# Kernel optimization log

Hardware: AMD Instinct MI355X
Metric: run time of the kernel (lower is better)

Reference implementation:

```python
import jax, jax.numpy as jnp
import numpy as np

B, S, V, D, L, H = 2, 512, 100300, 768, 12, 3072


def setup_inputs() -> dict:
    key = jax.random.key(0)
    ks = jax.random.split(key, 24)
    nrm = lambda k, shape, s=0.02: (jax.random.normal(k, shape, jnp.float32) * s)
    uni = lambda k, shape: jax.random.uniform(k, shape, jnp.float32)
    return {
        "tokens": jax.random.randint(ks[0], (B, S), 0, V, dtype=jnp.int32),
        "emb": nrm(ks[1], (V, D)),
        "ln0_g": jnp.ones((D,), jnp.float32), "ln0_b": jnp.zeros((D,), jnp.float32),
        "ln1_g": jnp.ones((L, D), jnp.float32), "ln1_b": jnp.zeros((L, D), jnp.float32),
        "ln2_g": jnp.ones((L, D), jnp.float32), "ln2_b": jnp.zeros((L, D), jnp.float32),
        "time_decay": nrm(ks[2], (L, D), 0.5),
        "time_first": nrm(ks[3], (L, D), 0.5),
        "tm_mu_k": uni(ks[4], (L, D)), "tm_mu_v": uni(ks[5], (L, D)), "tm_mu_r": uni(ks[6], (L, D)),
        "tm_Wk": nrm(ks[7], (L, D, D)), "tm_Wv": nrm(ks[8], (L, D, D)),
        "tm_Wr": nrm(ks[9], (L, D, D)), "tm_Wo": nrm(ks[10], (L, D, D)),
        "cm_mu_k": uni(ks[11], (L, D)), "cm_mu_r": uni(ks[12], (L, D)),
        "cm_Wk": nrm(ks[13], (L, D, H)), "cm_Wv": nrm(ks[14], (L, H, D)), "cm_Wr": nrm(ks[15], (L, D, D)),
        "lnf_g": jnp.ones((D,), jnp.float32), "lnf_b": jnp.zeros((D,), jnp.float32),
        "head": nrm(ks[16], (D, V)),
    }


def _ln(x, g, b, eps=1e-5):
    m = jnp.mean(x, axis=-1, keepdims=True)
    v = jnp.mean(jnp.square(x - m), axis=-1, keepdims=True)
    return (x - m) * jax.lax.rsqrt(v + eps) * g + b


def _shift(x):  # previous-token shift along seq axis, zeros at t=0; x: [B,S,D]
    return jnp.concatenate([jnp.zeros_like(x[:, :1]), x[:, :-1]], axis=1)


def _wkv(k, v, w, u):
    """RWKV-4 max-stabilized WKV linear recurrence. k,v: [B,S,D]; w,u: [D]."""
    decay = -jnp.exp(w)  # negative per-channel decay

    def step(carry, inp):
        p, a, b = carry
        kt, vt = inp
        ww = u + kt
        q = jnp.maximum(p, ww)
        e1 = jnp.exp(p - q)
        e2 = jnp.exp(ww - q)
        out = (e1 * a + e2 * vt) / (e1 * b + e2)
        ww2 = p + decay
        q2 = jnp.maximum(ww2, kt)
        e1 = jnp.exp(ww2 - q2)
        e2 = jnp.exp(kt - q2)
        return (q2, e1 * a + e2 * vt, e1 * b + e2), out

    kT = jnp.swapaxes(k, 0, 1)  # [S,B,D]
    vT = jnp.swapaxes(v, 0, 1)
    p0 = jnp.full((k.shape[0], k.shape[2]), -1e38, k.dtype)
    a0 = jnp.zeros_like(p0)
    b0 = jnp.zeros_like(p0)
    _, out = jax.lax.scan(step, (p0, a0, b0), (kT, vT))
    return jnp.swapaxes(out, 0, 1)  # [B,S,D]


def reference(tokens, emb, ln0_g, ln0_b, ln1_g, ln1_b, ln2_g, ln2_b,
              time_decay, time_first, tm_mu_k, tm_mu_v, tm_mu_r,
              tm_Wk, tm_Wv, tm_Wr, tm_Wo, cm_mu_k, cm_mu_r,
              cm_Wk, cm_Wv, cm_Wr, lnf_g, lnf_b, head):
    x = emb[tokens]                      # [B,S,D]
    x = _ln(x, ln0_g, ln0_b)
    n_layer = ln1_g.shape[0]
    for l in range(n_layer):
        # --- time mixing ---
        xx = _ln(x, ln1_g[l], ln1_b[l])
        sx = _shift(xx)
        xk = xx * tm_mu_k[l] + sx * (1.0 - tm_mu_k[l])
        xv = xx * tm_mu_v[l] + sx * (1.0 - tm_mu_v[l])
        xr = xx * tm_mu_r[l] + sx * (1.0 - tm_mu_r[l])
        r = jax.nn.sigmoid(jnp.einsum('bsd,de->bse', xr, tm_Wr[l]))
        k = jnp.einsum('bsd,de->bse', xk, tm_Wk[l])
        v = jnp.einsum('bsd,de->bse', xv, tm_Wv[l])
        wkv = _wkv(k, v, time_decay[l], time_first[l])
        x = x + jnp.einsum('bsd,de->bse', r * wkv, tm_Wo[l])
        # --- channel mixing ---
        xx = _ln(x, ln2_g[l], ln2_b[l])
        sx = _shift(xx)
        xk = xx * cm_mu_k[l] + sx * (1.0 - cm_mu_k[l])
        xr = xx * cm_mu_r[l] + sx * (1.0 - cm_mu_r[l])
        kk = jnp.square(jax.nn.relu(jnp.einsum('bsd,dh->bsh', xk, cm_Wk[l])))
        x = x + jax.nn.sigmoid(jnp.einsum('bsd,de->bse', xr, cm_Wr[l])) * jnp.einsum('bsh,hd->bsd', kk, cm_Wv[l])
    x = _ln(x, lnf_g, lnf_b)
    return jnp.einsum('bsd,dv->bsv', x, head)  # [B,S,V] logits
```

## Files before the change

### kernel.cpp

```cpp
#include <hip/hip_runtime.h>

typedef float f32x4v __attribute__((ext_vector_type(4)));
typedef __bf16 bf16x8 __attribute__((ext_vector_type(8)));

__device__ __forceinline__ ushort f2bf(float f) {
    unsigned u = __builtin_bit_cast(unsigned, f);
    return (ushort)((u + 0x7FFFu + ((u >> 16) & 1u)) >> 16);
}

__device__ __forceinline__ void gload16(const void* g, void* l) {
    __builtin_amdgcn_global_load_lds(
        (const __attribute__((address_space(1))) void*)g,
        (__attribute__((address_space(3))) void*)l, 16, 0, 0);
}

__global__ __launch_bounds__(256)
void prep_w(const float* __restrict__ Win, ushort* __restrict__ Wout,
            int K, int N, size_t sIn, size_t sOut)
{
    __shared__ float t[64][65];
    const float* W = Win + sIn * blockIdx.z;
    ushort* O = Wout + sOut * blockIdx.z;
    int n0 = blockIdx.x * 64, k0 = blockIdx.y * 64;
    int tid = threadIdx.x;
    int c = tid & 63, r4 = tid >> 6;
#pragma unroll
    for (int i = 0; i < 16; i++) {
        int rr = i * 4 + r4;
        int n = n0 + c;
        t[rr][c] = (n < N) ? W[(size_t)(k0 + rr) * N + n] : 0.f;
    }
    __syncthreads();
#pragma unroll
    for (int i = 0; i < 16; i++) {
        int nr = i * 4 + r4;
        O[(size_t)(n0 + nr) * K + k0 + c] = f2bf(t[c][nr]);
    }
}

__global__ __launch_bounds__(256)
void prep_dd(const float* __restrict__ W0, const float* __restrict__ W1,
             const float* __restrict__ W2, const float* __restrict__ W3,
             const float* __restrict__ W4,
             ushort* __restrict__ O0, ushort* __restrict__ O1,
             ushort* __restrict__ O2, ushort* __restrict__ O3,
             ushort* __restrict__ O4)
{
    __shared__ float t[64][65];
    const int z = blockIdx.z, wsel = z / 12, l = z % 12;
    const size_t DD = (size_t)768 * 768;
    const float* W = (wsel == 0 ? W0 : wsel == 1 ? W1 : wsel == 2 ? W2 : wsel == 3 ? W3 : W4) + DD * l;
    ushort* O = (wsel == 0 ? O0 : wsel == 1 ? O1 : wsel == 2 ? O2 : wsel == 3 ? O3 : O4) + DD * l;
    int n0 = blockIdx.x * 64, k0 = blockIdx.y * 64;
    int tid = threadIdx.x;
    int c = tid & 63, r4 = tid >> 6;
#pragma unroll
    for (int i = 0; i < 16; i++) {
        int rr = i * 4 + r4;
        t[rr][c] = W[(size_t)(k0 + rr) * 768 + n0 + c];
    }
    __syncthreads();
#pragma unroll
    for (int i = 0; i < 16; i++) {
        int nr = i * 4 + r4;
        O[(size_t)(n0 + nr) * 768 + k0 + c] = f2bf(t[c][nr]);
    }
}

template <int BM, int BN, int EPI>
__device__ __forceinline__
void gemm_body(const ushort* __restrict__ A, const ushort* __restrict__ B,
               float* __restrict__ C, ushort* __restrict__ Obf,
               const float* __restrict__ G,
               int N, int K, int mtiles, int bid, int tid,
               ushort* __restrict__ As, ushort* __restrict__ Bs)
{
    constexpr int WM = BM / 2, WN = BN / 2, MF = WM / 16, NF = WN / 16;
    const int mt = bid % mtiles, nt = bid / mtiles;
    const int m0 = mt * BM, n0 = nt * BN;
    const int w = tid >> 6, l = tid & 63;
    const int wr = w >> 1, wc = w & 1, g = l >> 4, lr = l & 15;
    const int lrow = l >> 3, lcol = ((l & 7) ^ lrow) * 8;

    auto stage = [&](int buf, int k0) {
#pragma unroll
        for (int i = 0; i < BM / 32; i++) {
            int rb = (i * 4 + w) * 8;
            gload16(A + (size_t)(m0 + rb + lrow) * K + k0 + lcol, &As[buf * BM * 64 + rb * 64]);
        }
#pragma unroll
        for (int i = 0; i < BN / 32; i++) {
            int rb = (i * 4 + w) * 8;
            gload16(B + (size_t)(n0 + rb + lrow) * K + k0 + lcol, &Bs[buf * BN * 64 + rb * 64]);
        }
    };

    f32x4v acc[MF][NF] = {};
    auto comp = [&](int buf) {
#pragma unroll
        for (int kk = 0; kk < 2; kk++) {
            bf16x8 af[MF], bfr[NF];
            const int sl = ((kk * 4 + g) ^ (lr & 7)) * 8;
#pragma unroll
            for (int mi = 0; mi < MF; mi++)
                af[mi] = *(const bf16x8*)&As[buf * BM * 64 + (wr * WM + mi * 16 + lr) * 64 + sl];
#pragma unroll
            for (int ni = 0; ni < NF; ni++)
                bfr[ni] = *(const bf16x8*)&Bs[buf * BN * 64 + (wc * WN + ni * 16 + lr) * 64 + sl];
#pragma unroll
            for (int mi = 0; mi < MF; mi++)
#pragma unroll
                for (int ni = 0; ni < NF; ni++)
                    acc[mi][ni] = __builtin_amdgcn_mfma_f32_16x16x32_bf16(
                        af[mi], bfr[ni], acc[mi][ni], 0, 0, 0);
        }
    };

    const int NS = K >> 6;
    stage(0, 0);
    __syncthreads();
    for (int s = 0; s < NS; s++) {
        if (s + 1 < NS) stage((s + 1) & 1, (s + 1) << 6);
        comp(s & 1);
        __syncthreads();
    }

#pragma unroll
    for (int mi = 0; mi < MF; mi++) {
        int row = m0 + wr * WM + mi * 16 + 4 * g;
#pragma unroll
        for (int ni = 0; ni < NF; ni++) {
            int col = n0 + wc * WN + ni * 16 + lr;
#pragma unroll
            for (int q = 0; q < 4; q++) {
                size_t idx = (size_t)(row + q) * N + col;
                float vv = acc[mi][ni][q];
                if constexpr (EPI == 0) {
                    C[idx] = vv;
                } else if constexpr (EPI == 1) {
                    C[idx] += vv;
                } else if constexpr (EPI == 2) {
                    float t = vv > 0.f ? vv : 0.f;
                    Obf[idx] = f2bf(t * t);
                } else {
                    float gt = 1.f / (1.f + __expf(-G[idx]));
                    C[idx] += gt * vv;
                }
            }
        }
    }
}

template <int BM, int BN, int EPI>
__global__ __launch_bounds__(256)
void gemm2(const ushort* __restrict__ Abase,
           const ushort* __restrict__ B0, const ushort* __restrict__ B1,
           const ushort* __restrict__ B2,
           float* __restrict__ Cbase, ushort* __restrict__ ObfBase,
           const float* __restrict__ Gbase,
           int M, int N, int K, int mtiles)
{
    __shared__ ushort As[2 * BM * 64];
    __shared__ ushort Bs[2 * BN * 64];
    const int z = blockIdx.z;
    const ushort* A = Abase + (size_t)z * M * K;
    const ushort* B = (z == 0) ? B0 : ((z == 1) ? B1 : B2);
    float* C = Cbase ? Cbase + (size_t)z * M * N : nullptr;
    ushort* Obf = ObfBase ? ObfBase + (size_t)z * M * N : nullptr;
    int bid = blockIdx.x;
    { int cpx = gridDim.x >> 3; bid = (bid & 7) * cpx + (bid >> 3); }
    gemm_body<BM, BN, EPI>(A, B, C, Obf, Gbase, N, K, mtiles, bid, threadIdx.x, As, Bs);
}

__global__ __launch_bounds__(256)
void gemm_ckcr(const ushort* __restrict__ xk, const ushort* __restrict__ xr,
               const ushort* __restrict__ ckT, const ushort* __restrict__ crT,
               ushort* __restrict__ hbuf, float* __restrict__ rrb)
{
    __shared__ ushort As[2 * 64 * 64];
    __shared__ ushort Bs[2 * 32 * 64];
    int bid = blockIdx.x;
    { int cpx = gridDim.x >> 3; bid = (bid & 7) * cpx + (bid >> 3); }
    if (bid < 1536)
        gemm_body<64, 32, 2>(xk, ckT, nullptr, hbuf, nullptr, 3072, 768, 16,
                             bid, threadIdx.x, As, Bs);
    else
        gemm_body<64, 32, 0>(xr, crT, rrb, nullptr, nullptr, 768, 768, 16,
                             bid - 1536, threadIdx.x, As, Bs);
}

__global__ __launch_bounds__(256, 4)
void head_gemm(const ushort* __restrict__ A, const ushort* __restrict__ B,
               float* __restrict__ C, int M, int N, int K, int mtiles)
{
    constexpr int WM = 64, WN = 64;
    __shared__ ushort As[2][128 * 32];
    __shared__ ushort Bs[2][128 * 32];

    int bid = blockIdx.x;
    { int cpx = gridDim.x >> 3; bid = (bid & 7) * cpx + (bid >> 3); }
    const int mt = bid % mtiles, nt = bid / mtiles;
    const int m0 = mt * 128, n0 = nt * 128;
    const int tid = threadIdx.x, w = tid >> 6, l = tid & 63;
    const int wr = w >> 1, wc = w & 1, g = l >> 4, lr = l & 15;
    const int lrow = l >> 2;
    const int lcol = ((l & 3) ^ (lrow & 3) ^ ((lrow >> 2) & 3)) * 8;

    auto stage = [&](int buf, int k0) {
#pragma unroll
        for (int i = 0; i < 2; i++) {
            int rg = i * 4 + w;
            gload16(A + (size_t)(m0 + rg * 16 + lrow) * K + k0 + lcol, &As[buf][rg * 512]);
        }
#pragma unroll
        for (int i = 0; i < 2; i++) {
            int rg = i * 4 + w;
            gload16(B + (size_t)(n0 + rg * 16 + lrow) * K + k0 + lcol, &Bs[buf][rg * 512]);
        }
    };

    f32x4v acc[4][4] = {};
    auto comp = [&](int buf) {
        bf16x8 af[4], bfr[4];
        const int sl = (g ^ (lr & 3) ^ ((lr >> 2) & 3)) * 8;
#pragma unroll
        for (int mi = 0; mi < 4; mi++)
            af[mi] = *(const bf16x8*)&As[buf][(wr * WM + mi * 16 + lr) * 32 + sl];
#pragma unroll
        for (int ni = 0; ni < 4; ni++)
            bfr[ni] = *(const bf16x8*)&Bs[buf][(wc * WN + ni * 16 + lr) * 32 + sl];
#pragma unroll
        for (int mi = 0; mi < 4; mi++)
#pragma unroll
            for (int ni = 0; ni < 4; ni++)
                acc[mi][ni] = __builtin_amdgcn_mfma_f32_16x16x32_bf16(
                    af[mi], bfr[ni], acc[mi][ni], 0, 0, 0);
    };

    const int NS = K / 32;
    stage(0, 0);
    __syncthreads();
    for (int s = 0; s < NS; s++) {
        if (s + 1 < NS) stage((s + 1) & 1, (s + 1) * 32);
        comp(s & 1);
        __syncthreads();
    }

#pragma unroll
    for (int mi = 0; mi < 4; mi++) {
        int row = m0 + wr * WM + mi * 16 + 4 * g;
#pragma unroll
        for (int ni = 0; ni < 4; ni++) {
            int col = n0 + wc * WN + ni * 16 + lr;
            if (col >= N) continue;
#pragma unroll
            for (int q = 0; q < 4; q++)
                C[(size_t)(row + q) * N + col] = acc[mi][ni][q];
        }
    }
}

__device__ __forceinline__ float4 blockReduce4(float4 v) {
#pragma unroll
    for (int off = 32; off; off >>= 1) {
        v.x += __shfl_down(v.x, off);
        v.y += __shfl_down(v.y, off);
        v.z += __shfl_down(v.z, off);
        v.w += __shfl_down(v.w, off);
    }
    __shared__ float4 red[4];
    int tid = threadIdx.x;
    if ((tid & 63) == 0) red[tid >> 6] = v;
    __syncthreads();
    float4 r = red[0];
    r.x += red[1].x + red[2].x + red[3].x;
    r.y += red[1].y + red[2].y + red[3].y;
    r.z += red[1].z + red[2].z + red[3].z;
    r.w += red[1].w + red[2].w + red[3].w;
    return r;
}

__global__ void embed_ln0(const int* __restrict__ tokens, const float* __restrict__ emb,
                          const float* __restrict__ g, const float* __restrict__ be,
                          float* __restrict__ x)
{
    int tau = blockIdx.x, tid = threadIdx.x;
    const float* e = emb + (size_t)tokens[tau] * 768;
    float a[3]; float s1 = 0, s2 = 0;
#pragma unroll
    for (int i = 0; i < 3; i++) {
        float av = e[tid + i * 256]; a[i] = av; s1 += av; s2 += av * av;
    }
    float4 r = blockReduce4(make_float4(s1, s2, 0.f, 0.f));
    const float inv = 1.f / 768.f;
    float m = r.x * inv, va = r.y * inv - m * m, rs = rsqrtf(va + 1e-5f);
#pragma unroll
    for (int i = 0; i < 3; i++) {
        int d = tid + i * 256;
        x[(size_t)tau * 768 + d] = (a[i] - m) * rs * g[d] + be[d];
    }
}

__global__ void ln_mix_tm(const float* __restrict__ x,
                          const float* __restrict__ g, const float* __restrict__ be,
                          const float* __restrict__ muk, const float* __restrict__ muv,
                          const float* __restrict__ mur,
                          ushort* __restrict__ xk, ushort* __restrict__ xv,
                          ushort* __restrict__ xr)
{
    int tau = blockIdx.x, tid = threadIdx.x;
    bool hasp = (tau & 511) != 0;
    const float* xp = x + (size_t)tau * 768;
    const float* pp = xp - 768;
    float a[3], b[3]; float s1 = 0, s2 = 0, s3 = 0, s4 = 0;
#pragma unroll
    for (int i = 0; i < 3; i++) {
        int d = tid + i * 256;
        float av = xp[d]; a[i] = av; s1 += av; s2 += av * av;
        float bv = hasp ? pp[d] : 0.f; b[i] = bv; s3 += bv; s4 += bv * bv;
    }
    float4 r = blockReduce4(make_float4(s1, s2, s3, s4));
    const float inv = 1.f / 768.f;
    float m1 = r.x * inv, va = r.y * inv - m1 * m1, rs1 = rsqrtf(va + 1e-5f);
    float m2 = r.z * inv, vb = r.w * inv - m2 * m2, rs2 = rsqrtf(vb + 1e-5f);
#pragma unroll
    for (int i = 0; i < 3; i++) {
        int d = tid + i * 256;
        float gg = g[d], bb = be[d];
        float xx = (a[i] - m1) * rs1 * gg + bb;
        float sx = hasp ? ((b[i] - m2) * rs2 * gg + bb) : 0.f;
        size_t o = (size_t)tau * 768 + d;
        float mk = muk[d]; xk[o] = f2bf(xx * mk + sx * (1.f - mk));
        float mv = muv[d]; xv[o] = f2bf(xx * mv + sx * (1.f - mv));
        float mr = mur[d]; xr[o] = f2bf(xx * mr + sx * (1.f - mr));
    }
}

__global__ void ln_mix_cm(const float* __restrict__ x,
                          const float* __restrict__ g, const float* __restrict__ be,
                          const float* __restrict__ muk, const float* __restrict__ mur,
                          ushort* __restrict__ xk, ushort* __restrict__ xr)
{
    int tau = blockIdx.x, tid = threadIdx.x;
    bool hasp = (tau & 511) != 0;
    const float* xp = x + (size_t)tau * 768;
    const float* pp = xp - 768;
    float a[3], b[3]; float s1 = 0, s2 = 0, s3 = 0, s4 = 0;
#pragma unroll
    for (int i = 0; i < 3; i++) {
        int d = tid + i * 256;
        float av = xp[d]; a[i] = av; s1 += av; s2 += av * av;
        float bv = hasp ? pp[d] : 0.f; b[i] = bv; s3 += bv; s4 += bv * bv;
    }
    float4 r = blockReduce4(make_float4(s1, s2, s3, s4));
    const float inv = 1.f / 768.f;
    float m1 = r.x * inv, va = r.y * inv - m1 * m1, rs1 = rsqrtf(va + 1e-5f);
    float m2 = r.z * inv, vb = r.w * inv - m2 * m2, rs2 = rsqrtf(vb + 1e-5f);
#pragma unroll
    for (int i = 0; i < 3; i++) {
        int d = tid + i * 256;
        float gg = g[d], bb = be[d];
        float xx = (a[i] - m1) * rs1 * gg + bb;
        float sx = hasp ? ((b[i] - m2) * rs2 * gg + bb) : 0.f;
        size_t o = (size_t)tau * 768 + d;
        float mk = muk[d]; xk[o] = f2bf(xx * mk + sx * (1.f - mk));
        float mr = mur[d]; xr[o] = f2bf(xx * mr + sx * (1.f - mr));
    }
}

__global__ void ln_final(const float* __restrict__ x,
                         const float* __restrict__ g, const float* __restrict__ be,
                         ushort* __restrict__ xf)
{
    int tau = blockIdx.x, tid = threadIdx.x;
    const float* xp = x + (size_t)tau * 768;
    float a[3]; float s1 = 0, s2 = 0;
#pragma unroll
    for (int i = 0; i < 3; i++) {
        float av = xp[tid + i * 256]; a[i] = av; s1 += av; s2 += av * av;
    }
    float4 r = blockReduce4(make_float4(s1, s2, 0.f, 0.f));
    const float inv = 1.f / 768.f;
    float m = r.x * inv, va = r.y * inv - m * m, rs = rsqrtf(va + 1e-5f);
#pragma unroll
    for (int i = 0; i < 3; i++) {
        int d = tid + i * 256;
        xf[(size_t)tau * 768 + d] = f2bf((a[i] - m) * rs * g[d] + be[d]);
    }
}

__global__ __launch_bounds__(256)
void wkv_par(const float* __restrict__ kk, const float* __restrict__ vv,
             const float* __restrict__ rr, const float* __restrict__ td,
             const float* __restrict__ tf, ushort* __restrict__ out)
{
    const int blk = blockIdx.x, tid = threadIdx.x;
    const int b = blk / 48, chb = blk % 48;
    const int seg = tid >> 4, ch = tid & 15;
    const int d = chb * 16 + ch;
    const size_t base = (size_t)b * 512 * 768 + d;
    const size_t soff = (size_t)seg * 32 * 768;
    const float w = -__expf(td[d]);
    const float u = tf[d];
    const int CH = 8;

    __shared__ float sp[240], sa[240], sb[240];
    __shared__ float pp[256], pa[256], pb[256];

    if (seg < 15) {
        float p = -1e38f, aa = 0.f, bb = 0.f;
        const float* kp = kk + base + soff;
        const float* vp = vv + base + soff;
        float k8[CH], v8[CH], kn[CH], vn[CH];
#pragma unroll
        for (int j = 0; j < CH; j++) { k8[j] = kp[j * 768]; v8[j] = vp[j * 768]; }
        for (int c = 0; c < 32 / CH; c++) {
            if (c + 1 < 32 / CH) {
                size_t o = (size_t)(c + 1) * CH * 768;
#pragma unroll
                for (int j = 0; j < CH; j++) { kn[j] = kp[o + j * 768]; vn[j] = vp[o + j * 768]; }
            }
#pragma unroll
            for (int j = 0; j < CH; j++) {
                float kt = k8[j], vt = v8[j];
                float ww2 = p + w;
                float q2 = fmaxf(ww2, kt);
                float f1 = __expf(ww2 - q2), f2 = __expf(kt - q2);
                aa = f1 * aa + f2 * vt;
                bb = f1 * bb + f2;
                p = q2;
            }
#pragma unroll
            for (int j = 0; j < CH; j++) { k8[j] = kn[j]; v8[j] = vn[j]; }
        }
        sp[seg * 16 + ch] = p; sa[seg * 16 + ch] = aa; sb[seg * 16 + ch] = bb;
    }
    __syncthreads();

    if (tid < 16) {
        const float shift = 32.f * w;
        float P = -1e38f, A = 0.f, Bc = 0.f;
#pragma unroll
        for (int s = 0; s < 16; s++) {
            pp[s * 16 + tid] = P; pa[s * 16 + tid] = A; pb[s * 16 + tid] = Bc;
            if (s < 15) {
                float ps = P + shift;
                float sps = sp[s * 16 + tid];
                float q = fmaxf(ps, sps);
                float e1 = __expf(ps - q), e2 = __expf(sps - q);
                A  = e1 * A  + e2 * sa[s * 16 + tid];
                Bc = e1 * Bc + e2 * sb[s * 16 + tid];
                P = q;
            }
        }
    }
    __syncthreads();

    {
        float p = pp[tid], aa = pa[tid], bb = pb[tid];
        const float* kp = kk + base + soff;
        const float* vp = vv + base + soff;
        const float* rp = rr + base + soff;
        ushort* op = out + base + soff;
        float k8[CH], v8[CH], r8[CH], kn[CH], vn[CH], rn[CH];
#pragma unroll
        for (int j = 0; j < CH; j++) {
            k8[j] = kp[j * 768]; v8[j] = vp[j * 768]; r8[j] = rp[j * 768];
        }
        for (int c = 0; c < 32 / CH; c++) {
            if (c + 1 < 32 / CH) {
                size_t o = (size_t)(c + 1) * CH * 768;
#pragma unroll
                for (int j = 0; j < CH; j++) {
                    kn[j] = kp[o + j * 768]; vn[j] = vp[o + j * 768]; rn[j] = rp[o + j * 768];
                }
            }
#pragma unroll
            for (int j = 0; j < CH; j++) {
                float kt = k8[j], vt = v8[j];
                float ww = u + kt;
                float q = fmaxf(p, ww);
                float e1 = __expf(p - q), e2 = __expf(ww - q);
                float o = (e1 * aa + e2 * vt) / (e1 * bb + e2);
                float sr = 1.f / (1.f + __expf(-r8[j]));
                op[(size_t)(c * CH + j) * 768] = f2bf(sr * o);
                float ww2 = p + w;
                float q2 = fmaxf(ww2, kt);
                float f1 = __expf(ww2 - q2), f2 = __expf(kt - q2);
                aa = f1 * aa + f2 * vt;
                bb = f1 * bb + f2;
                p = q2;
            }
#pragma unroll
            for (int j = 0; j < CH; j++) { k8[j] = kn[j]; v8[j] = vn[j]; r8[j] = rn[j]; }
        }
    }
}

extern "C" void kernel_launch(void* const* d_in, const int* in_sizes, int n_in,
                              void* d_out, int out_size, void* d_ws, size_t ws_size,
                              hipStream_t stream)
{
    const int V = 100300, D = 768, L = 12, H = 3072;
    const int T = 1024;
    const int Vp = 100352;

    const int*   tokens     = (const int*)d_in[0];
    const float* emb        = (const float*)d_in[1];
    const float* ln0_g      = (const float*)d_in[2];
    const float* ln0_b      = (const float*)d_in[3];
    const float* ln1_g      = (const float*)d_in[4];
    const float* ln1_b      = (const float*)d_in[5];
    const float* ln2_g      = (const float*)d_in[6];
    const float* ln2_b      = (const float*)d_in[7];
    const float* time_decay = (const float*)d_in[8];
    const float* time_first = (const float*)d_in[9];
    const float* tm_mu_k    = (const float*)d_in[10];
    const float* tm_mu_v    = (const float*)d_in[11];
    const float* tm_mu_r    = (const float*)d_in[12];
    const float* tm_Wk      = (const float*)d_in[13];
    const float* tm_Wv      = (const float*)d_in[14];
    const float* tm_Wr      = (const float*)d_in[15];
    const float* tm_Wo      = (const float*)d_in[16];
    const float* cm_mu_k    = (const float*)d_in[17];
    const float* cm_mu_r    = (const float*)d_in[18];
    const float* cm_Wk      = (const float*)d_in[19];
    const float* cm_Wv      = (const float*)d_in[20];
    const float* cm_Wr      = (const float*)d_in[21];
    const float* lnf_g      = (const float*)d_in[22];
    const float* lnf_b      = (const float*)d_in[23];
    const float* head       = (const float*)d_in[24];

    char* wp = (char*)d_ws;
    auto alloc = [&](size_t bytes) -> char* {
        char* p = wp; wp += (bytes + 255) & ~(size_t)255; return p;
    };
    const size_t eDD = (size_t)L * D * D;
    const size_t eDH = (size_t)L * D * H;
    ushort* wkT = (ushort*)alloc(eDD * 2);
    ushort* wvT = (ushort*)alloc(eDD * 2);
    ushort* wrT = (ushort*)alloc(eDD * 2);
    ushort* woT = (ushort*)alloc(eDD * 2);
    ushort* ckT = (ushort*)alloc(eDH * 2);
    ushort* cvT = (ushort*)alloc(eDH * 2);
    ushort* crT = (ushort*)alloc(eDD * 2);
    ushort* hdT = (ushort*)alloc((size_t)Vp * D * 2);

    float*  x    = (float*)alloc((size_t)T * D * 4);
    ushort* xkb  = (ushort*)alloc((size_t)3 * T * D * 2);
    float*  kvr  = (float*)alloc((size_t)3 * T * D * 4);
    ushort* rwkv = (ushort*)alloc((size_t)T * D * 2);
    ushort* hbuf = (ushort*)alloc((size_t)T * H * 2);
    float*  rrb  = (float*)alloc((size_t)T * D * 4);
    ushort* xf   = (ushort*)alloc((size_t)T * D * 2);

    prep_dd<<<dim3(12, 12, 60), 256, 0, stream>>>(tm_Wk, tm_Wv, tm_Wr, tm_Wo, cm_Wr,
                                                  wkT, wvT, wrT, woT, crT);
    prep_w<<<dim3(H / 64, D / 64, L), 256, 0, stream>>>(cm_Wk, ckT, D, H, (size_t)D * H, (size_t)D * H);
    prep_w<<<dim3(D / 64, H / 64, L), 256, 0, stream>>>(cm_Wv, cvT, H, D, (size_t)D * H, (size_t)D * H);
    prep_w<<<dim3(Vp / 64, D / 64, 1), 256, 0, stream>>>(head, hdT, D, V, 0, 0);

    embed_ln0<<<T, 256, 0, stream>>>(tokens, emb, ln0_g, ln0_b, x);

    for (int l = 0; l < L; l++) {
        ln_mix_tm<<<T, 256, 0, stream>>>(x, ln1_g + l * D, ln1_b + l * D,
                                         tm_mu_k + l * D, tm_mu_v + l * D, tm_mu_r + l * D,
                                         xkb, xkb + (size_t)T * D, xkb + (size_t)2 * T * D);

        gemm2<64, 32, 0><<<dim3(384, 1, 3), 256, 0, stream>>>(
            xkb, wkT + l * (size_t)D * D, wvT + l * (size_t)D * D, wrT + l * (size_t)D * D,
            kvr, nullptr, nullptr, T, D, D, 16);

        wkv_par<<<96, 256, 0, stream>>>(kvr, kvr + (size_t)T * D, kvr + (size_t)2 * T * D,
                                        time_decay + l * D, time_first + l * D, rwkv);

        gemm2<64, 32, 1><<<dim3(384, 1, 1), 256, 0, stream>>>(
            rwkv, woT + l * (size_t)D * D, nullptr, nullptr,
            x, nullptr, nullptr, T, D, D, 16);

        ln_mix_cm<<<T, 256, 0, stream>>>(x, ln2_g + l * D, ln2_b + l * D,
                                         cm_mu_k + l * D, cm_mu_r + l * D,
                                         xkb, xkb + (size_t)T * D);

        gemm_ckcr<<<1920, 256, 0, stream>>>(xkb, xkb + (size_t)T * D,
                                            ckT + l * (size_t)D * H, crT + l * (size_t)D * D,
                                            hbuf, rrb);

        gemm2<64, 32, 3><<<dim3(384, 1, 1), 256, 0, stream>>>(
            hbuf, cvT + l * (size_t)D * H, nullptr, nullptr,
            x, nullptr, rrb, T, D, H, 16);
    }

    ln_final<<<T, 256, 0, stream>>>(x, lnf_g, lnf_b, xf);

    head_gemm<<<8 * (Vp / 128), 256, 0, stream>>>(xf, hdT, (float*)d_out, T, V, D, 8);
}
```

Measured before the change: 1.875 ms.

## Rewrite head GEMM with 256x256 tiles, 8 waves, and quarter-tile staged pipeline

```diff
diff --git a/kernel.cpp b/kernel.cpp
--- a/kernel.cpp
+++ b/kernel.cpp
@@ -189,73 +189,94 @@
                              bid - 1536, threadIdx.x, As, Bs);
 }
 
-__global__ __launch_bounds__(256, 4)
-void head_gemm(const ushort* __restrict__ A, const ushort* __restrict__ B,
-               float* __restrict__ C, int M, int N, int K, int mtiles)
-{
-    constexpr int WM = 64, WN = 64;
-    __shared__ ushort As[2][128 * 32];
-    __shared__ ushort Bs[2][128 * 32];
+#define HG_NT 12
+__global__ __launch_bounds__(512, 2)
+void head_gemm8(const ushort* __restrict__ Ag, const ushort* __restrict__ Bg,
+                float* __restrict__ C, int N)
+{
+    __shared__ ushort As[2][256 * 64];
+    __shared__ ushort Bs[2][256 * 64];
 
     int bid = blockIdx.x;
     { int cpx = gridDim.x >> 3; bid = (bid & 7) * cpx + (bid >> 3); }
-    const int mt = bid % mtiles, nt = bid / mtiles;
-    const int m0 = mt * 128, n0 = nt * 128;
+    const int mt = bid % 4, nt = bid / 4;
+    const int m0 = mt * 256, n0 = nt * 256;
     const int tid = threadIdx.x, w = tid >> 6, l = tid & 63;
-    const int wr = w >> 1, wc = w & 1, g = l >> 4, lr = l & 15;
-    const int lrow = l >> 2;
-    const int lcol = ((l & 3) ^ (lrow & 3) ^ ((lrow >> 2) & 3)) * 8;
-
-    auto stage = [&](int buf, int k0) {
-#pragma unroll
-        for (int i = 0; i < 2; i++) {
-            int rg = i * 4 + w;
-            gload16(A + (size_t)(m0 + rg * 16 + lrow) * K + k0 + lcol, &As[buf][rg * 512]);
-        }
-#pragma unroll
-        for (int i = 0; i < 2; i++) {
-            int rg = i * 4 + w;
-            gload16(B + (size_t)(n0 + rg * 16 + lrow) * K + k0 + lcol, &Bs[buf][rg * 512]);
+    const int wr = w >> 2, wc = w & 3, g = l >> 4, lr = l & 15;
+    const int lrow = l >> 3, lcol = ((l & 7) ^ lrow) * 8;
+
+    auto stageH = [&](int H) {
+        const int tau = H >> 2, part = H & 3, buf = tau & 1;
+        const int k0 = tau * 64;
+        const int half = (part >> 1) * 128;
+        ushort* dst;
+        const ushort* src;
+        int rbase;
+        if (part & 1) { dst = &Bs[buf][half * 64]; src = Bg; rbase = n0; }
+        else          { dst = &As[buf][half * 64]; src = Ag; rbase = m0; }
+#pragma unroll
+        for (int j = 0; j < 2; j++) {
+            int o = j * 8 + w;
+            gload16(src + (size_t)(rbase + half + o * 8 + lrow) * 768 + k0 + lcol,
+                    dst + o * 8 * 64);
         }
     };
 
-    f32x4v acc[4][4] = {};
-    auto comp = [&](int buf) {
-        bf16x8 af[4], bfr[4];
-        const int sl = (g ^ (lr & 3) ^ ((lr >> 2) & 3)) * 8;
-#pragma unroll
-        for (int mi = 0; mi < 4; mi++)
-            af[mi] = *(const bf16x8*)&As[buf][(wr * WM + mi * 16 + lr) * 32 + sl];
-#pragma unroll
-        for (int ni = 0; ni < 4; ni++)
-            bfr[ni] = *(const bf16x8*)&Bs[buf][(wc * WN + ni * 16 + lr) * 32 + sl];
-#pragma unroll
-        for (int mi = 0; mi < 4; mi++)
-#pragma unroll
-            for (int ni = 0; ni < 4; ni++)
-                acc[mi][ni] = __builtin_amdgcn_mfma_f32_16x16x32_bf16(
-                    af[mi], bfr[ni], acc[mi][ni], 0, 0, 0);
-    };
-
-    const int NS = K / 32;
-    stage(0, 0);
-    __syncthreads();
-    for (int s = 0; s < NS; s++) {
-        if (s + 1 < NS) stage((s + 1) & 1, (s + 1) * 32);
-        comp(s & 1);
-        __syncthreads();
-    }
-
-#pragma unroll
-    for (int mi = 0; mi < 4; mi++) {
-        int row = m0 + wr * WM + mi * 16 + 4 * g;
+    f32x4v acc[8][4] = {};
+
+#pragma unroll
+    for (int H = 0; H < 4; H++) stageH(H);
+
+    for (int t = 0; t < HG_NT; t++) {
+        const int buf = t & 1;
+#pragma unroll
+        for (int q = 0; q < 4; q++) {
+            __builtin_amdgcn_sched_barrier(0);
+            int H = 4 * t + q + 4;
+            if (H < 4 * HG_NT) stageH(H);
+            if (q == 0) {
+                if (t < HG_NT - 1) asm volatile("s_waitcnt vmcnt(2)" ::: "memory");
+                else               asm volatile("s_waitcnt vmcnt(0)" ::: "memory");
+            }
+            __builtin_amdgcn_s_barrier();
+            __builtin_amdgcn_sched_barrier(0);
+            __builtin_amdgcn_s_setprio(1);
+            {
+                const int mq = q >> 1, nq = q & 1;
+#pragma unroll
+                for (int kk = 0; kk < 2; kk++) {
+                    const int sl = ((kk * 4 + g) ^ (lr & 7)) * 8;
+                    bf16x8 af[4], bfr[2];
+#pragma unroll
+                    for (int i = 0; i < 4; i++)
+                        af[i] = *(const bf16x8*)&As[buf][(wr * 128 + (mq * 4 + i) * 16 + lr) * 64 + sl];
+#pragma unroll
+                    for (int j = 0; j < 2; j++)
+                        bfr[j] = *(const bf16x8*)&Bs[buf][(wc * 64 + (nq * 2 + j) * 16 + lr) * 64 + sl];
+#pragma unroll
+                    for (int i = 0; i < 4; i++)
+#pragma unroll
+                        for (int j = 0; j < 2; j++)
+                            acc[mq * 4 + i][nq * 2 + j] = __builtin_amdgcn_mfma_f32_16x16x32_bf16(
+                                af[i], bfr[j], acc[mq * 4 + i][nq * 2 + j], 0, 0, 0);
+                }
+            }
+            __builtin_amdgcn_s_setprio(0);
+            __builtin_amdgcn_sched_barrier(0);
+            __builtin_amdgcn_s_barrier();
+        }
+    }
+
+#pragma unroll
+    for (int mi = 0; mi < 8; mi++) {
+        int row = m0 + wr * 128 + mi * 16 + 4 * g;
 #pragma unroll
         for (int ni = 0; ni < 4; ni++) {
-            int col = n0 + wc * WN + ni * 16 + lr;
+            int col = n0 + wc * 64 + ni * 16 + lr;
             if (col >= N) continue;
 #pragma unroll
-            for (int q = 0; q < 4; q++)
-                C[(size_t)(row + q) * N + col] = acc[mi][ni][q];
+            for (int qq = 0; qq < 4; qq++)
+                C[(size_t)(row + qq) * N + col] = acc[mi][ni][qq];
         }
     }
 }
@@ -593,5 +614,5 @@
 
     ln_final<<<T, 256, 0, stream>>>(x, lnf_g, lnf_b, xf);
 
-    head_gemm<<<8 * (Vp / 128), 256, 0, stream>>>(xf, hdT, (float*)d_out, T, V, D, 8);
-}
+    head_gemm8<<<4 * (Vp / 256), 512, 0, stream>>>(xf, hdT, (float*)d_out, V);
+}
```

After: 1.980 ms. 5.6% more time.

## Software-pipeline head GEMM with split-K half-plane staging and explicit waitcnts

Applied to the files above, without the earlier changes.

```diff
diff --git a/kernel.cpp b/kernel.cpp
--- a/kernel.cpp
+++ b/kernel.cpp
@@ -189,69 +189,92 @@
                              bid - 1536, threadIdx.x, As, Bs);
 }
 
-__global__ __launch_bounds__(256, 4)
-void head_gemm(const ushort* __restrict__ A, const ushort* __restrict__ B,
-               float* __restrict__ C, int M, int N, int K, int mtiles)
-{
-    constexpr int WM = 64, WN = 64;
-    __shared__ ushort As[2][128 * 32];
-    __shared__ ushort Bs[2][128 * 32];
+#define HNT 12
+__global__ __launch_bounds__(256, 2)
+void head_gemmP(const ushort* __restrict__ Ag, const ushort* __restrict__ Bg,
+                float* __restrict__ C, int N)
+{
+    __shared__ ushort As[2][2][128 * 32];
+    __shared__ ushort Bs[2][2][128 * 32];
 
     int bid = blockIdx.x;
     { int cpx = gridDim.x >> 3; bid = (bid & 7) * cpx + (bid >> 3); }
-    const int mt = bid % mtiles, nt = bid / mtiles;
+    const int mt = bid % 8, nt = bid / 8;
     const int m0 = mt * 128, n0 = nt * 128;
     const int tid = threadIdx.x, w = tid >> 6, l = tid & 63;
     const int wr = w >> 1, wc = w & 1, g = l >> 4, lr = l & 15;
-    const int lrow = l >> 2;
-    const int lcol = ((l & 3) ^ (lrow & 3) ^ ((lrow >> 2) & 3)) * 8;
-
-    auto stage = [&](int buf, int k0) {
-#pragma unroll
-        for (int i = 0; i < 2; i++) {
-            int rg = i * 4 + w;
-            gload16(A + (size_t)(m0 + rg * 16 + lrow) * K + k0 + lcol, &As[buf][rg * 512]);
-        }
-#pragma unroll
-        for (int i = 0; i < 2; i++) {
-            int rg = i * 4 + w;
-            gload16(B + (size_t)(n0 + rg * 16 + lrow) * K + k0 + lcol, &Bs[buf][rg * 512]);
+    const int srow = l >> 2;
+    const int sslot = (l & 3) ^ ((l >> 2) & 3) ^ ((l >> 4) & 3);
+
+    auto stageP = [&](int tau, int kh, bool isB) {
+        if (tau >= HNT) return;
+        const int buf = tau & 1, k0 = tau * 64 + kh * 32;
+        ushort* plane = isB ? &Bs[buf][kh][0] : &As[buf][kh][0];
+        const ushort* src = isB ? Bg : Ag;
+        const int rbase = isB ? n0 : m0;
+#pragma unroll
+        for (int j = 0; j < 2; j++) {
+            int rc = (j * 4 + w) * 16;
+            gload16(src + (size_t)(rbase + rc + srow) * 768 + k0 + sslot * 8,
+                    plane + rc * 32);
         }
     };
 
     f32x4v acc[4][4] = {};
-    auto comp = [&](int buf) {
-        bf16x8 af[4], bfr[4];
-        const int sl = (g ^ (lr & 3) ^ ((lr >> 2) & 3)) * 8;
-#pragma unroll
-        for (int mi = 0; mi < 4; mi++)
-            af[mi] = *(const bf16x8*)&As[buf][(wr * WM + mi * 16 + lr) * 32 + sl];
-#pragma unroll
-        for (int ni = 0; ni < 4; ni++)
-            bfr[ni] = *(const bf16x8*)&Bs[buf][(wc * WN + ni * 16 + lr) * 32 + sl];
-#pragma unroll
-        for (int mi = 0; mi < 4; mi++)
-#pragma unroll
-            for (int ni = 0; ni < 4; ni++)
-                acc[mi][ni] = __builtin_amdgcn_mfma_f32_16x16x32_bf16(
-                    af[mi], bfr[ni], acc[mi][ni], 0, 0, 0);
-    };
-
-    const int NS = K / 32;
-    stage(0, 0);
-    __syncthreads();
-    for (int s = 0; s < NS; s++) {
-        if (s + 1 < NS) stage((s + 1) & 1, (s + 1) * 32);
-        comp(s & 1);
-        __syncthreads();
+
+    stageP(0, 0, false); stageP(0, 0, true);
+    stageP(0, 1, false); stageP(0, 1, true);
+    stageP(1, 0, false); stageP(1, 0, true);
+    asm volatile("s_waitcnt vmcnt(4)" ::: "memory");
+    __builtin_amdgcn_sched_barrier(0);
+    __builtin_amdgcn_s_barrier();
+
+    for (int t = 0; t < HNT; t++) {
+        const int buf = t & 1;
+#pragma unroll
+        for (int kh = 0; kh < 2; kh++) {
+            bf16x8 af[4], bf4[4];
+#pragma unroll
+            for (int mi = 0; mi < 4; mi++) {
+                int row = wr * 64 + mi * 16 + lr;
+                int sl = (g ^ (lr & 3) ^ ((lr >> 2) & 3)) * 8;
+                af[mi] = *(const bf16x8*)&As[buf][kh][row * 32 + sl];
+            }
+#pragma unroll
+            for (int ni = 0; ni < 4; ni++) {
+                int row = wc * 64 + ni * 16 + lr;
+                int sl = (g ^ (lr & 3) ^ ((lr >> 2) & 3)) * 8;
+                bf4[ni] = *(const bf16x8*)&Bs[buf][kh][row * 32 + sl];
+            }
+            if (kh == 0) { stageP(t + 1, 1, false); stageP(t + 1, 1, true); }
+            else         { stageP(t + 2, 0, false); stageP(t + 2, 0, true); }
+            __builtin_amdgcn_sched_barrier(0);
+            __builtin_amdgcn_s_barrier();
+            asm volatile("s_waitcnt lgkmcnt(0)" ::: "memory");
+            __builtin_amdgcn_sched_barrier(0);
+            __builtin_amdgcn_s_setprio(1);
+#pragma unroll
+            for (int mi = 0; mi < 4; mi++)
+#pragma unroll
+                for (int ni = 0; ni < 4; ni++)
+                    acc[mi][ni] = __builtin_amdgcn_mfma_f32_16x16x32_bf16(
+                        af[mi], bf4[ni], acc[mi][ni], 0, 0, 0);
+            __builtin_amdgcn_s_setprio(0);
+            if (kh == 1) {
+                if (t < HNT - 2)       asm volatile("s_waitcnt vmcnt(4)" ::: "memory");
+                else if (t == HNT - 2) asm volatile("s_waitcnt vmcnt(0)" ::: "memory");
+            }
+            __builtin_amdgcn_sched_barrier(0);
+            __builtin_amdgcn_s_barrier();
+        }
     }
 
 #pragma unroll
     for (int mi = 0; mi < 4; mi++) {
-        int row = m0 + wr * WM + mi * 16 + 4 * g;
+        int row = m0 + wr * 64 + mi * 16 + 4 * g;
 #pragma unroll
         for (int ni = 0; ni < 4; ni++) {
-            int col = n0 + wc * WN + ni * 16 + lr;
+            int col = n0 + wc * 64 + ni * 16 + lr;
             if (col >= N) continue;
 #pragma unroll
             for (int q = 0; q < 4; q++)
@@ -593,5 +616,5 @@
 
     ln_final<<<T, 256, 0, stream>>>(x, lnf_g, lnf_b, xf);
 
-    head_gemm<<<8 * (Vp / 128), 256, 0, stream>>>(xf, hdT, (float*)d_out, T, V, D, 8);
-}
+    head_gemmP<<<8 * (Vp / 128), 256, 0, stream>>>(xf, hdT, (float*)d_out, V);
+}
```

After: 1.907 ms. About the same (+1.7%).
